# Performance work log

Hardware: AMD Instinct MI355X
Metric: run time of the kernel (lower is better)

Reference implementation:

```python
import jax, jax.numpy as jnp
import numpy as np

N_NODES = 100000
N_EDGES = 1600000
FEAT = 512
CLS = 64
HID = 200  # each hop layer output width; 3 hops -> 600 concat


def spmm(row, col, vals, x):
    # out[r] = sum_{e: row[e]==r} vals[e] * x[col[e]]  -- sparse A @ x
    return jax.ops.segment_sum(x[col] * vals[:, None], row, num_segments=x.shape[0])


def setup_inputs() -> dict:
    key = jax.random.key(0)
    ks = jax.random.split(key, 12)
    adj_index = jax.random.randint(ks[0], (2, N_EDGES), 0, N_NODES, dtype=jnp.int64)
    # scale like a normalized adjacency (~1/avg_degree) to keep powers stable
    adj_values = jax.random.uniform(ks[1], (N_EDGES,), dtype=jnp.float32) * (1.0 / 16.0)
    features = jax.random.normal(ks[2], (N_NODES, FEAT), dtype=jnp.float32)
    s1 = (2.0 / (FEAT + HID)) ** 0.5
    s2 = (2.0 / (3 * HID + HID)) ** 0.5
    sf = (2.0 / (3 * HID + CLS)) ** 0.5
    W1 = jax.random.normal(ks[3], (3, FEAT, HID), dtype=jnp.float32) * s1
    b1 = jax.random.normal(ks[4], (3, HID), dtype=jnp.float32) * 0.01
    W2 = jax.random.normal(ks[5], (3, 3 * HID, HID), dtype=jnp.float32) * s2
    b2 = jax.random.normal(ks[6], (3, HID), dtype=jnp.float32) * 0.01
    Wfc = jax.random.normal(ks[7], (3 * HID, CLS), dtype=jnp.float32) * sf
    bfc = jax.random.normal(ks[8], (CLS,), dtype=jnp.float32) * 0.01
    return {"adj_index": adj_index, "adj_values": adj_values, "features": features,
            "W1": W1, "b1": b1, "W2": W2, "b2": b2, "Wfc": Wfc, "bfc": bfc}


def reference(adj_index, adj_values, features, W1, b1, W2, b2, Wfc, bfc):
    # Inference mode: dropout is identity.
    row, col = adj_index[0], adj_index[1]
    # upper (sparse) layers: linear + bias + relu, then (iterations-1) spmm hops
    outs1 = []
    for i in range(3):  # iterations = i + 1
        h = jax.nn.relu(features @ W1[i] + b1[i][None, :])
        for _ in range(i):
            h = spmm(row, col, adj_values, h)
        outs1.append(h)
    abstract1 = jnp.concatenate(outs1, axis=1)  # [N, 600]
    # bottom (dense) layers: linear, (iterations-1) spmm hops, then + bias
    outs2 = []
    for i in range(3):
        h = abstract1 @ W2[i]
        for _ in range(i):
            h = spmm(row, col, adj_values, h)
        h = h + b2[i][None, :]
        outs2.append(h)
    abstract2 = jnp.concatenate(outs2, axis=1)  # [N, 600]
    node_emb = abstract2 @ Wfc + bfc  # [N, CLS]
    predictions = jax.nn.log_softmax(node_emb, axis=1)
    return node_emb, predictions
```

## Files before the change

### kernel.cpp

```cpp
#include <hip/hip_runtime.h>

typedef unsigned short u16;
typedef unsigned int u32;
typedef __attribute__((ext_vector_type(8))) short short8;
typedef __attribute__((ext_vector_type(4))) float f32x4;
typedef __attribute__((ext_vector_type(4))) u32 u32x4;
typedef __attribute__((ext_vector_type(2))) u32 u32x2;

#define NN 100000
#define PAD 640

__device__ __forceinline__ float b2f(u16 u) {
    union { u32 i; float f; } v; v.i = ((u32)u) << 16; return v.f;
}
__device__ __forceinline__ u16 f2b(float f) {
    union { float f; u32 i; } v; v.f = f;
    u32 x = v.i;
    return (u16)((x + 0x7FFFu + ((x >> 16) & 1u)) >> 16);
}
__device__ __forceinline__ u32 pack2(float lo, float hi) {
    return (u32)f2b(lo) | ((u32)f2b(hi) << 16);
}
__device__ __forceinline__ float rdf(const void* p, size_t i, int f) {
    return f ? ((const float*)p)[i] : b2f(((const u16*)p)[i]);
}
__device__ __forceinline__ void gload16(const u16* g, u16* l) {
    __builtin_amdgcn_global_load_lds(
        (const __attribute__((address_space(1))) void*)g,
        (__attribute__((address_space(3))) void*)l, 16, 0, 0);
}

__global__ void probe_k(const int* __restrict__ idx,
                        const void* avals, const void* feats, const void* W1,
                        const void* b1, const void* W2, const void* b2,
                        const void* Wfc, const void* bfc,
                        int* __restrict__ flags) {
    if (blockIdx.x != 0 || threadIdx.x >= 64) return;
    int lane = threadIdx.x;
    int v0 = idx[2 * lane + 1];
    int v1 = idx[2 * (lane + 64) + 1];
    int ok = (v0 == 0 && v1 == 0);
    int allz = __all(ok);
    if (lane == 0) flags[0] = allz ? 1 : 0;
    const void* ts[8] = {avals, feats, W1, b1, W2, b2, Wfc, bfc};
    const int ns[8] = {256, 256, 256, 128, 256, 128, 256, 32};
    for (int t = 0; t < 8; ++t) {
        const u16* p = (const u16*)ts[t];
        int n = ns[t], bad = 0;
        for (int i = lane; i < n; i += 64) {
            int e = (p[2 * i] >> 7) & 0xFF;
            if (e >= 133) bad++;
        }
        for (int off = 32; off; off >>= 1) bad += __shfl_xor(bad, off, 64);
        if (lane == 0) flags[1 + t] = (bad * 8 >= n) ? 1 : 0;
    }
}

__device__ __forceinline__ int load_row(const int* idx, int E, int f, int e) {
    return f ? idx[2 * e] : idx[e];
}
__device__ __forceinline__ int load_col(const int* idx, int E, int f, int e) {
    return f ? idx[2 * E + 2 * e] : idx[E + e];
}

__global__ void featconv_k(const void* __restrict__ src, u16* __restrict__ dst,
                           const int* __restrict__ flags) {
    int i = blockIdx.x * 256 + threadIdx.x;
    if (i >= NN * 64) return;
    int f = flags[2];
    size_t b = (size_t)i * 8;
    short8 o;
    if (f) {
        const float* sf = (const float*)src + b;
        f32x4 x0 = *(const f32x4*)sf;
        f32x4 x1 = *(const f32x4*)(sf + 4);
#pragma unroll
        for (int q = 0; q < 4; ++q) {
            o[q] = (short)f2b(x0[q]);
            o[q + 4] = (short)f2b(x1[q]);
        }
    } else {
        o = *(const short8*)((const u16*)src + b);
    }
    *(short8*)(dst + b) = o;
}

__global__ void prep_k(const void* __restrict__ W1, const void* __restrict__ W2,
                       const void* __restrict__ Wfc,
                       const void* __restrict__ b1, const void* __restrict__ b2,
                       const void* __restrict__ bfc,
                       u16* __restrict__ w1t, u16* __restrict__ w2t,
                       u16* __restrict__ wfct, float* __restrict__ biasf,
                       const int* __restrict__ flags) {
    int i = blockIdx.x * 256 + threadIdx.x;
    int job = blockIdx.y;
    if (job == 0) {
        if (i >= 640 * 512) return;
        int n = i >> 9, k = i & 511;
        float v = 0.f;
        if (n < 600) {
            int ib = n / 200, c = n % 200;
            v = rdf(W1, (size_t)ib * 102400 + (size_t)k * 200 + c, flags[3]);
        }
        w1t[i] = f2b(v);
    } else if (job == 1) {
        if (i >= 640 * 640) return;
        int n = i / 640, k = i % 640;
        float v = 0.f;
        if (n < 600 && k < 600) {
            int ib = n / 200, c = n % 200;
            v = rdf(W2, (size_t)ib * 120000 + (size_t)k * 200 + c, flags[5]);
        }
        w2t[i] = f2b(v);
    } else if (job == 2) {
        if (i >= 64 * 640) return;
        int n = i / 640, k = i % 640;
        float v = 0.f;
        if (k < 600) v = rdf(Wfc, (size_t)k * 64 + n, flags[7]);
        wfct[i] = f2b(v);
    } else if (job == 3) {
        if (i < 600) biasf[i] = rdf(b1, i, flags[4]);
        else if (i < 1200) biasf[i] = rdf(b2, i - 600, flags[6]);
        else if (i < 1264) biasf[i] = rdf(bfc, i - 1200, flags[8]);
    } else {
        if (i >= 64) return;
        int fb2 = flags[6], fwf = flags[7];
        float s = rdf(bfc, i, flags[8]);
        for (int k = 0; k < 200; ++k)
            s += rdf(b2, k, fb2) * rdf(Wfc, (size_t)k * 64 + i, fwf);
        biasf[1280 + i] = s;
    }
}

__device__ __forceinline__ int pad8(int c) { return (c + 7) & ~7; }

__global__ void count_k(const int* __restrict__ idx, int E, const int* __restrict__ flags,
                        int* __restrict__ counts) {
    int e = blockIdx.x * 256 + threadIdx.x;
    if (e >= E) return;
    int r = load_row(idx, E, flags[0], e);
    if ((u32)r >= NN) return;
    atomicAdd(&counts[r], 1);
}

__global__ void chunksum_k(const int* __restrict__ counts, int* __restrict__ chsum) {
    __shared__ int sm[256];
    int c = blockIdx.x, t = threadIdx.x;
    int base = c * 1024, s = 0;
    for (int i = t; i < 1024; i += 256) {
        int g = base + i;
        if (g < NN) s += pad8(counts[g]);
    }
    sm[t] = s; __syncthreads();
    for (int off = 128; off; off >>= 1) {
        if (t < off) sm[t] += sm[t + off];
        __syncthreads();
    }
    if (t == 0) chsum[c] = sm[0];
}

__global__ void chscan_k(const int* __restrict__ chsum, int nch, int* __restrict__ choff,
                         int* __restrict__ row_ptr, int E) {
    if (threadIdx.x == 0 && blockIdx.x == 0) {
        int run = 0;
        for (int c = 0; c < nch; ++c) { choff[c] = run; run += chsum[c]; }
        row_ptr[NN] = run;
    }
}

__global__ __launch_bounds__(1024) void scan_k(const int* __restrict__ counts,
                                               const int* __restrict__ choff,
                                               int* __restrict__ row_ptr,
                                               int* __restrict__ cursor) {
    __shared__ int sm[1024];
    int c = blockIdx.x, t = threadIdx.x;
    int g = c * 1024 + t;
    int v = (g < NN) ? pad8(counts[g]) : 0;
    sm[t] = v;
    __syncthreads();
    for (int off = 1; off < 1024; off <<= 1) {
        int add = (t >= off) ? sm[t - off] : 0;
        __syncthreads();
        sm[t] += add;
        __syncthreads();
    }
    if (g < NN) {
        int ex = choff[c] + sm[t] - v;
        row_ptr[g] = ex;
        cursor[g] = ex;
    }
}

__global__ void scatter_k(const int* __restrict__ idx, const void* __restrict__ avals, int E,
                          const int* __restrict__ flags, int* __restrict__ cursor,
                          int* __restrict__ edges) {
    int e = blockIdx.x * 256 + threadIdx.x;
    if (e >= E) return;
    int f = flags[0];
    int r = load_row(idx, E, f, e);
    if ((u32)r >= NN) return;
    int c = load_col(idx, E, f, e);
    if ((u32)c >= NN) c = 0;
    int p = atomicAdd(&cursor[r], 1);
    edges[2 * p] = c;
    ((float*)edges)[2 * p + 1] = rdf(avals, e, flags[1]);
}

__global__ void padfill_k(const int* __restrict__ cursor, const int* __restrict__ row_ptr,
                          int* __restrict__ edges) {
    int r = blockIdx.x * 256 + threadIdx.x;
    if (r >= NN) return;
    int p = cursor[r], e = row_ptr[r + 1];
    for (; p < e; ++p) {
        edges[2 * p] = 0;
        ((float*)edges)[2 * p + 1] = 0.f;
    }
}

__global__ __launch_bounds__(256) void gemm128_k(
    const u16* __restrict__ A, const u16* __restrict__ Bt,
    u16* __restrict__ C, float* __restrict__ Cf,
    const float* __restrict__ bias, int bias_n, int relu,
    int M, int K, int lda, int ldc) {
    __shared__ u16 As[128 * 32];
    __shared__ u16 Bs[128 * 32];
    const int tid = threadIdx.x;
    const int wave = tid >> 6, lane = tid & 63;

    const int nwg = gridDim.x;
    const int q = nwg >> 3, r8 = nwg & 7;
    const int xcd = blockIdx.x & 7, lo = blockIdx.x >> 3;
    const int wg = (xcd < r8 ? xcd * (q + 1) : r8 * (q + 1) + (xcd - r8) * q) + lo;
    const int bmi = wg / 5, bni = wg - bmi * 5;
    const int bm = bmi * 128, bn = bni * 128;

    const int wrow = (wave >> 1) * 64, wcol = (wave & 1) * 64;
    const int l15 = lane & 15, l4 = lane >> 4;
    f32x4 acc[4][4] = {};

    const int c0 = wave * 2;
    const int rowA0 = c0 * 16 + (lane >> 2);
    const int rowA1 = rowA0 + 16;
    const int colE = (lane & 3) * 8;
    int gr0 = bm + rowA0; if (gr0 >= M) gr0 = M - 1;
    int gr1 = bm + rowA1; if (gr1 >= M) gr1 = M - 1;
    const u16* a0p = A + (size_t)gr0 * lda + colE;
    const u16* a1p = A + (size_t)gr1 * lda + colE;
    const u16* b0p = Bt + (size_t)(bn + rowA0) * K + colE;
    const u16* b1p = Bt + (size_t)(bn + rowA1) * K + colE;
    u16* lA0 = As + c0 * 512;
    u16* lA1 = As + c0 * 512 + 512;
    u16* lB0 = Bs + c0 * 512;
    u16* lB1 = Bs + c0 * 512 + 512;

    for (int k0 = 0; k0 < K; k0 += 32) {
        __syncthreads();
        gload16(a0p + k0, lA0);
        gload16(a1p + k0, lA1);
        gload16(b0p + k0, lB0);
        gload16(b1p + k0, lB1);
        __syncthreads();
        short8 af[4], bf[4];
#pragma unroll
        for (int t = 0; t < 4; ++t) {
            af[t] = *(const short8*)&As[(wrow + t * 16 + l15) * 32 + l4 * 8];
            bf[t] = *(const short8*)&Bs[(wcol + t * 16 + l15) * 32 + l4 * 8];
        }
#pragma unroll
        for (int mi = 0; mi < 4; ++mi)
#pragma unroll
            for (int ni = 0; ni < 4; ++ni)
                acc[mi][ni] = __builtin_amdgcn_mfma_f32_16x16x32_bf16(
                    af[mi], bf[ni], acc[mi][ni], 0, 0, 0);
    }

#pragma unroll
    for (int mi = 0; mi < 4; ++mi)
#pragma unroll
        for (int ni = 0; ni < 4; ++ni)
#pragma unroll
            for (int r4 = 0; r4 < 4; ++r4) {
                int row = bm + wrow + mi * 16 + l4 * 4 + r4;
                int col = bn + wcol + ni * 16 + l15;
                if (row < M) {
                    float v = acc[mi][ni][r4];
                    if (bias && col < bias_n) v += bias[col];
                    if (relu) v = fmaxf(v, 0.0f);
                    if (C) C[(size_t)row * ldc + col] = f2b(v);
                    if (Cf) Cf[(size_t)row * ldc + col] = v;
                }
            }
}

__global__ __launch_bounds__(256) void fc64_k(
    const u16* __restrict__ A0, const u16* __restrict__ A1,
    const u16* __restrict__ Bt,
    float* __restrict__ out_ne, float* __restrict__ out_pred,
    const float* __restrict__ bias, int M, int K, int lda) {
    __shared__ __align__(16) char ldsbuf[128 * 64 * 4];
    u16* As = (u16*)ldsbuf;
    u16* Bs = (u16*)(ldsbuf + 8192);
    float* smC = (float*)ldsbuf;

    const int tid = threadIdx.x;
    const int wave = tid >> 6, lane = tid & 63;
    const int bm = blockIdx.x * 128;
    const int wrow = (wave >> 1) * 64, wcol = (wave & 1) * 32;
    const int l15 = lane & 15, l4 = lane >> 4;
    f32x4 acc[4][2] = {};

    const int colE = (lane & 3) * 8;
    int gr0 = bm + wave * 32 + (lane >> 2); if (gr0 >= M) gr0 = M - 1;
    int gr1 = bm + wave * 32 + 16 + (lane >> 2); if (gr1 >= M) gr1 = M - 1;
    const u16* a0p0 = A0 + (size_t)gr0 * lda + colE;
    const u16* a0p1 = A1 + (size_t)gr0 * lda + colE;
    const u16* a1p0 = A0 + (size_t)gr1 * lda + colE;
    const u16* a1p1 = A1 + (size_t)gr1 * lda + colE;
    const u16* bp = Bt + (size_t)(wave * 16 + (lane >> 2)) * K + colE;
    u16* lA0 = As + wave * 1024;
    u16* lA1 = As + wave * 1024 + 512;
    u16* lB = Bs + wave * 512;

    for (int k0 = 0; k0 < K; k0 += 32) {
        const bool in0 = (k0 + colE) < 200;
        const u16* pa0 = in0 ? a0p0 : a0p1;
        const u16* pa1 = in0 ? a1p0 : a1p1;
        __syncthreads();
        gload16(pa0 + k0, lA0);
        gload16(pa1 + k0, lA1);
        gload16(bp + k0, lB);
        __syncthreads();
        short8 af[4], bf[2];
#pragma unroll
        for (int t = 0; t < 4; ++t)
            af[t] = *(const short8*)&As[(wrow + t * 16 + l15) * 32 + l4 * 8];
#pragma unroll
        for (int t = 0; t < 2; ++t)
            bf[t] = *(const short8*)&Bs[(wcol + t * 16 + l15) * 32 + l4 * 8];
#pragma unroll
        for (int mi = 0; mi < 4; ++mi)
#pragma unroll
            for (int ni = 0; ni < 2; ++ni)
                acc[mi][ni] = __builtin_amdgcn_mfma_f32_16x16x32_bf16(
                    af[mi], bf[ni], acc[mi][ni], 0, 0, 0);
    }

    __syncthreads();
#pragma unroll
    for (int mi = 0; mi < 4; ++mi)
#pragma unroll
        for (int ni = 0; ni < 2; ++ni)
#pragma unroll
            for (int r4 = 0; r4 < 4; ++r4) {
                int rl = wrow + mi * 16 + l4 * 4 + r4;
                int col = wcol + ni * 16 + l15;
                int row = bm + rl;
                float v = acc[mi][ni][r4] + bias[col];
                smC[rl * 64 + col] = v;
                if (row < M) out_ne[(size_t)row * 64 + col] = v;
            }
    __syncthreads();

    const int rl = tid >> 1, half = tid & 1;
    const int row = bm + rl;
    float vv[32];
#pragma unroll
    for (int k = 0; k < 32; ++k) {
        int c = half * 32 + ((k + rl) & 31);
        vv[k] = smC[rl * 64 + c];
    }
    float m = vv[0];
#pragma unroll
    for (int k = 1; k < 32; ++k) m = fmaxf(m, vv[k]);
    m = fmaxf(m, __shfl_xor(m, 1, 64));
    float s = 0.f;
#pragma unroll
    for (int k = 0; k < 32; ++k) s += expf(vv[k] - m);
    s += __shfl_xor(s, 1, 64);
    float lg = m + logf(s);
    if (row < M) {
#pragma unroll
        for (int k = 0; k < 32; ++k) {
            int c = half * 32 + ((k + rl) & 31);
            out_pred[(size_t)row * 64 + c] = vv[k] - lg;
        }
    }
}

__global__ __launch_bounds__(256) void spmm400_k(
    const int* __restrict__ row_ptr, const int* __restrict__ edges,
    const u16* __restrict__ X, u16* __restrict__ Y1, u16* __restrict__ Yt,
    const float* __restrict__ bias1) {
    int r = blockIdx.x * 4 + (threadIdx.x >> 6);
    if (r >= NN) return;
    int lane = threadIdx.x & 63;
    int s = row_ptr[r], e = row_ptr[r + 1];
    if (s < 0) s = 0;
    if (e < s) e = s;
    float a[8] = {0.f, 0.f, 0.f, 0.f, 0.f, 0.f, 0.f, 0.f};
    const bool act = lane < 50;
    const u32* xl = (const u32*)X + lane * 4;
    for (int i = s; i < e; i += 8) {
        int cc[8]; float vv[8];
#pragma unroll
        for (int j = 0; j < 4; ++j) {
            u32x4 p = *(const u32x4*)(edges + 2 * (size_t)(i + 2 * j));
            union { u32 u; float f; } w0, w1;
            cc[2 * j] = (int)p[0];     w0.u = p[1];
            cc[2 * j + 1] = (int)p[2]; w1.u = p[3];
            vv[2 * j] = w0.f; vv[2 * j + 1] = w1.f;
        }
        if (act) {
            u32x4 g[8];
#pragma unroll
            for (int j = 0; j < 8; ++j) {
                u32 c = (u32)cc[j]; if (c >= NN) c = 0;
                g[j] = *(const u32x4*)(xl + (size_t)c * 320);
            }
#pragma unroll
            for (int j = 0; j < 8; ++j) {
                float v = vv[j];
#pragma unroll
                for (int q = 0; q < 4; ++q) {
                    union { u32 i; float f; } lo, hi;
                    lo.i = g[j][q] << 16; hi.i = g[j][q] & 0xffff0000u;
                    a[2 * q] = fmaf(v, lo.f, a[2 * q]);
                    a[2 * q + 1] = fmaf(v, hi.f, a[2 * q + 1]);
                }
            }
        }
    }
    if (bias1 && lane < 25) {
#pragma unroll
        for (int q = 0; q < 8; ++q) a[q] += bias1[lane * 8 + q];
    }
    u32x4 o;
    o[0] = pack2(a[0], a[1]); o[1] = pack2(a[2], a[3]);
    o[2] = pack2(a[4], a[5]); o[3] = pack2(a[6], a[7]);
    if (lane < 25) {
        *(u32x4*)((u32*)Y1 + (size_t)r * 320 + lane * 4) = o;
    } else if (lane < 50) {
        *(u32x4*)((u32*)Yt + (size_t)r * 100 + (lane - 25) * 4) = o;
    }
}

__global__ __launch_bounds__(256) void spmm200_k(
    const int* __restrict__ row_ptr, const int* __restrict__ edges,
    const u16* __restrict__ X, int ldx,
    u16* __restrict__ Y, int ldy,
    const float* __restrict__ bias) {
    int r = blockIdx.x * 4 + (threadIdx.x >> 6);
    if (r >= NN) return;
    int lane = threadIdx.x & 63;
    int s = row_ptr[r], e = row_ptr[r + 1];
    if (s < 0) s = 0;
    if (e < s) e = s;
    float a[4] = {0.f, 0.f, 0.f, 0.f};
    const bool act = lane < 50;
    const int ldxw = ldx >> 1, ldyw = ldy >> 1;
    const u32* xl = (const u32*)X + lane * 2;
    for (int i = s; i < e; i += 8) {
        int cc[8]; float vv[8];
#pragma unroll
        for (int j = 0; j < 4; ++j) {
            u32x4 p = *(const u32x4*)(edges + 2 * (size_t)(i + 2 * j));
            union { u32 u; float f; } w0, w1;
            cc[2 * j] = (int)p[0];     w0.u = p[1];
            cc[2 * j + 1] = (int)p[2]; w1.u = p[3];
            vv[2 * j] = w0.f; vv[2 * j + 1] = w1.f;
        }
        if (act) {
            u32x2 g[8];
#pragma unroll
            for (int j = 0; j < 8; ++j) {
                u32 c = (u32)cc[j]; if (c >= NN) c = 0;
                g[j] = *(const u32x2*)(xl + (size_t)c * ldxw);
            }
#pragma unroll
            for (int j = 0; j < 8; ++j) {
                float v = vv[j];
#pragma unroll
                for (int q = 0; q < 2; ++q) {
                    union { u32 i; float f; } lo, hi;
                    lo.i = g[j][q] << 16; hi.i = g[j][q] & 0xffff0000u;
                    a[2 * q] = fmaf(v, lo.f, a[2 * q]);
                    a[2 * q + 1] = fmaf(v, hi.f, a[2 * q + 1]);
                }
            }
        }
    }
    if (bias && act) {
#pragma unroll
        for (int q = 0; q < 4; ++q) a[q] += bias[lane * 4 + q];
    }
    if (act) {
        u32x2 o;
        o[0] = pack2(a[0], a[1]); o[1] = pack2(a[2], a[3]);
        *(u32x2*)((u32*)Y + (size_t)r * ldyw + lane * 2) = o;
    }
}

__global__ void copypad_k(const u16* __restrict__ src, u16* __restrict__ dst) {
    int i = blockIdx.x * 256 + threadIdx.x;
    if (i >= NN * 120) return;
    int r = i / 120, c = i % 120;
    if (c < 100)
        ((u32*)dst)[(size_t)r * 320 + c] = ((const u32*)src)[(size_t)r * 320 + c];
    else
        ((u32*)dst)[(size_t)r * 320 + 300 + (c - 100)] = 0u;
}

extern "C" void kernel_launch(void* const* d_in, const int* in_sizes, int n_in,
                              void* d_out, int out_size, void* d_ws, size_t ws_size,
                              hipStream_t stream) {
    const int* adj_idx = (const int*)d_in[0];
    const void* adj_vals = d_in[1];
    const void* feats = d_in[2];
    const void* W1 = d_in[3];
    const void* b1 = d_in[4];
    const void* W2 = d_in[5];
    const void* b2 = d_in[6];
    const void* Wfc = d_in[7];
    const void* bfc = d_in[8];
    const int E = in_sizes[1];
    (void)n_in; (void)out_size; (void)ws_size;

    char* ws = (char*)d_ws;
    size_t off = 0;
    auto alloc = [&](size_t b) { size_t o = off; off += (b + 255) & ~(size_t)255; return o; };
    u16* buf0 = (u16*)(ws + alloc((size_t)NN * PAD * 2));
    u16* buf1 = (u16*)(ws + alloc((size_t)NN * PAD * 2));
    u16* hop = (u16*)(ws + alloc((size_t)NN * 200 * 2));
    u16* w1t = (u16*)(ws + alloc((size_t)640 * 512 * 2));
    u16* w2t = (u16*)(ws + alloc((size_t)640 * 640 * 2));
    u16* wfct = (u16*)(ws + alloc((size_t)64 * 640 * 2));
    float* biasf = (float*)(ws + alloc(1344 * 4));
    int* counts = (int*)(ws + alloc((size_t)NN * 4));
    int* cursor = (int*)(ws + alloc((size_t)NN * 4));
    int* row_ptr = (int*)(ws + alloc((size_t)(NN + 1) * 4));
    int* chsum = (int*)(ws + alloc(4096));
    int* choff = (int*)(ws + alloc(4096));
    int* flags = (int*)(ws + alloc(256));
    int* edgesS = (int*)(ws + alloc(((size_t)E + 8 * (size_t)NN) * 8));

    u16* featsB = buf1;
    float* out_ne = (float*)d_out;
    float* out_pred = out_ne + (size_t)NN * 64;

    probe_k<<<1, 64, 0, stream>>>(adj_idx, adj_vals, feats, W1, b1, W2, b2, Wfc, bfc, flags);
    featconv_k<<<(NN * 64 + 255) / 256, 256, 0, stream>>>(feats, featsB, flags);
    dim3 gp(1600, 5);
    prep_k<<<gp, 256, 0, stream>>>(W1, W2, Wfc, b1, b2, bfc, w1t, w2t, wfct, biasf, flags);

    hipMemsetAsync(counts, 0, NN * 4, stream);
    count_k<<<(E + 255) / 256, 256, 0, stream>>>(adj_idx, E, flags, counts);
    const int NCH = (NN + 1023) / 1024;
    chunksum_k<<<NCH, 256, 0, stream>>>(counts, chsum);
    chscan_k<<<1, 64, 0, stream>>>(chsum, NCH, choff, row_ptr, E);
    scan_k<<<NCH, 1024, 0, stream>>>(counts, choff, row_ptr, cursor);
    scatter_k<<<(E + 255) / 256, 256, 0, stream>>>(adj_idx, adj_vals, E, flags, cursor, edgesS);
    padfill_k<<<(NN + 255) / 256, 256, 0, stream>>>(cursor, row_ptr, edgesS);

    const int NWG = ((NN + 127) / 128) * 5;
    gemm128_k<<<NWG, 256, 0, stream>>>(featsB, w1t, buf0, nullptr, biasf, 600, 1, NN, 512, 512, PAD);
    copypad_k<<<(NN * 120 + 255) / 256, 256, 0, stream>>>(buf0, buf1);
    spmm400_k<<<(NN + 3) / 4, 256, 0, stream>>>(row_ptr, edgesS,
                                                buf0 + 200, buf1 + 200, hop, nullptr);
    spmm200_k<<<(NN + 3) / 4, 256, 0, stream>>>(row_ptr, edgesS,
                                                hop, 200, buf1 + 400, PAD, nullptr);
    gemm128_k<<<NWG, 256, 0, stream>>>(buf1, w2t, buf0, nullptr, nullptr, 0, 0, NN, PAD, PAD, PAD);
    spmm400_k<<<(NN + 3) / 4, 256, 0, stream>>>(row_ptr, edgesS,
                                                buf0 + 200, buf1 + 200, hop, biasf + 800);
    spmm200_k<<<(NN + 3) / 4, 256, 0, stream>>>(row_ptr, edgesS,
                                                hop, 200, buf1 + 400, PAD, biasf + 1000);
    fc64_k<<<(NN + 127) / 128, 256, 0, stream>>>(buf0, buf1, wfct, out_ne, out_pred,
                                                 biasf + 1280, NN, PAD, PAD);
}
```

Measured before the change: 1.566 ms.

## Fuse feature conversion and pad copy into first GEMM

Drops the standalone fp32-to-bf16 feature conversion kernel and the copypad kernel. A new first-layer GEMM reads the raw features, converts them to bf16 in registers before staging them in LDS, and writes the relu output to both buffers for the needed column ranges. This removes a full write and reread of the 100k×512 bf16 feature matrix plus one 600-column copy pass. The cost is a GEMM whose A-operand load is now synchronous and unpipelined, with doubled global reads in fp32, and a scalar per-element epilogue store.

```diff
diff --git a/kernel.cpp b/kernel.cpp
--- a/kernel.cpp
+++ b/kernel.cpp
@@ -63,28 +63,6 @@
     return f ? idx[2 * E + 2 * e] : idx[E + e];
 }
 
-__global__ void featconv_k(const void* __restrict__ src, u16* __restrict__ dst,
-                           const int* __restrict__ flags) {
-    int i = blockIdx.x * 256 + threadIdx.x;
-    if (i >= NN * 64) return;
-    int f = flags[2];
-    size_t b = (size_t)i * 8;
-    short8 o;
-    if (f) {
-        const float* sf = (const float*)src + b;
-        f32x4 x0 = *(const f32x4*)sf;
-        f32x4 x1 = *(const f32x4*)(sf + 4);
-#pragma unroll
-        for (int q = 0; q < 4; ++q) {
-            o[q] = (short)f2b(x0[q]);
-            o[q + 4] = (short)f2b(x1[q]);
-        }
-    } else {
-        o = *(const short8*)((const u16*)src + b);
-    }
-    *(short8*)(dst + b) = o;
-}
-
 __global__ void prep_k(const void* __restrict__ W1, const void* __restrict__ W2,
                        const void* __restrict__ Wfc,
                        const void* __restrict__ b1, const void* __restrict__ b2,
@@ -217,6 +195,101 @@
     }
 }
 
+__global__ __launch_bounds__(256) void gemm1_k(
+    const void* __restrict__ A, const u16* __restrict__ Bt,
+    u16* __restrict__ C, u16* __restrict__ Cc,
+    const float* __restrict__ bias, const int* __restrict__ flags,
+    int M, int K, int lda, int ldc) {
+    __shared__ u16 As[128 * 32];
+    __shared__ u16 Bs[128 * 32];
+    const int tid = threadIdx.x;
+    const int wave = tid >> 6, lane = tid & 63;
+
+    const int nwg = gridDim.x;
+    const int q = nwg >> 3, r8 = nwg & 7;
+    const int xcd = blockIdx.x & 7, lo = blockIdx.x >> 3;
+    const int wg = (xcd < r8 ? xcd * (q + 1) : r8 * (q + 1) + (xcd - r8) * q) + lo;
+    const int bmi = wg / 5, bni = wg - bmi * 5;
+    const int bm = bmi * 128, bn = bni * 128;
+
+    const int wrow = (wave >> 1) * 64, wcol = (wave & 1) * 64;
+    const int l15 = lane & 15, l4 = lane >> 4;
+    f32x4 acc[4][4] = {};
+
+    const int ff = flags[2];
+    const int c0 = wave * 2;
+    const int rowA0 = c0 * 16 + (lane >> 2);
+    const int rowA1 = rowA0 + 16;
+    const int colE = (lane & 3) * 8;
+    int gr0 = bm + rowA0; if (gr0 >= M) gr0 = M - 1;
+    int gr1 = bm + rowA1; if (gr1 >= M) gr1 = M - 1;
+    const float* a0f = (const float*)A + (size_t)gr0 * lda + colE;
+    const float* a1f = (const float*)A + (size_t)gr1 * lda + colE;
+    const u16* a0h = (const u16*)A + (size_t)gr0 * lda + colE;
+    const u16* a1h = (const u16*)A + (size_t)gr1 * lda + colE;
+    const u16* b0p = Bt + (size_t)(bn + rowA0) * K + colE;
+    const u16* b1p = Bt + (size_t)(bn + rowA1) * K + colE;
+    u16* lA0 = &As[rowA0 * 32 + colE];
+    u16* lA1 = &As[rowA1 * 32 + colE];
+    u16* lB0 = Bs + c0 * 512;
+    u16* lB1 = Bs + c0 * 512 + 512;
+
+    for (int k0 = 0; k0 < K; k0 += 32) {
+        short8 av0, av1;
+        if (ff) {
+            f32x4 x0 = *(const f32x4*)(a0f + k0);
+            f32x4 x1 = *(const f32x4*)(a0f + k0 + 4);
+            f32x4 y0 = *(const f32x4*)(a1f + k0);
+            f32x4 y1 = *(const f32x4*)(a1f + k0 + 4);
+#pragma unroll
+            for (int t = 0; t < 4; ++t) {
+                av0[t] = (short)f2b(x0[t]); av0[t + 4] = (short)f2b(x1[t]);
+                av1[t] = (short)f2b(y0[t]); av1[t + 4] = (short)f2b(y1[t]);
+            }
+        } else {
+            av0 = *(const short8*)(a0h + k0);
+            av1 = *(const short8*)(a1h + k0);
+        }
+        __syncthreads();
+        *(short8*)lA0 = av0;
+        *(short8*)lA1 = av1;
+        gload16(b0p + k0, lB0);
+        gload16(b1p + k0, lB1);
+        __syncthreads();
+        short8 af[4], bf[4];
+#pragma unroll
+        for (int t = 0; t < 4; ++t) {
+            af[t] = *(const short8*)&As[(wrow + t * 16 + l15) * 32 + l4 * 8];
+            bf[t] = *(const short8*)&Bs[(wcol + t * 16 + l15) * 32 + l4 * 8];
+        }
+#pragma unroll
+        for (int mi = 0; mi < 4; ++mi)
+#pragma unroll
+            for (int ni = 0; ni < 4; ++ni)
+                acc[mi][ni] = __builtin_amdgcn_mfma_f32_16x16x32_bf16(
+                    af[mi], bf[ni], acc[mi][ni], 0, 0, 0);
+    }
+
+#pragma unroll
+    for (int mi = 0; mi < 4; ++mi)
+#pragma unroll
+        for (int ni = 0; ni < 4; ++ni)
+#pragma unroll
+            for (int r4 = 0; r4 < 4; ++r4) {
+                int row = bm + wrow + mi * 16 + l4 * 4 + r4;
+                int col = bn + wcol + ni * 16 + l15;
+                if (row < M) {
+                    float v = acc[mi][ni][r4];
+                    if (col < 600) v += bias[col];
+                    v = fmaxf(v, 0.0f);
+                    u16 b = f2b(v);
+                    C[(size_t)row * ldc + col] = b;
+                    if (col < 200 || col >= 600)
+                        Cc[(size_t)row * ldc + col] = b;
+                }
+            }
+}
+
 __global__ __launch_bounds__(256) void gemm128_k(
     const u16* __restrict__ A, const u16* __restrict__ Bt,
     u16* __restrict__ C, float* __restrict__ Cf,
@@ -500,16 +573,6 @@
     }
 }
 
-__global__ void copypad_k(const u16* __restrict__ src, u16* __restrict__ dst) {
-    int i = blockIdx.x * 256 + threadIdx.x;
-    if (i >= NN * 120) return;
-    int r = i / 120, c = i % 120;
-    if (c < 100)
-        ((u32*)dst)[(size_t)r * 320 + c] = ((const u32*)src)[(size_t)r * 320 + c];
-    else
-        ((u32*)dst)[(size_t)r * 320 + 300 + (c - 100)] = 0u;
-}
-
 extern "C" void kernel_launch(void* const* d_in, const int* in_sizes, int n_in,
                               void* d_out, int out_size, void* d_ws, size_t ws_size,
                               hipStream_t stream) {
@@ -543,12 +606,10 @@
     int* flags = (int*)(ws + alloc(256));
     int* edgesS = (int*)(ws + alloc(((size_t)E + 8 * (size_t)NN) * 8));
 
-    u16* featsB = buf1;
     float* out_ne = (float*)d_out;
     float* out_pred = out_ne + (size_t)NN * 64;
 
     probe_k<<<1, 64, 0, stream>>>(adj_idx, adj_vals, feats, W1, b1, W2, b2, Wfc, bfc, flags);
-    featconv_k<<<(NN * 64 + 255) / 256, 256, 0, stream>>>(feats, featsB, flags);
     dim3 gp(1600, 5);
     prep_k<<<gp, 256, 0, stream>>>(W1, W2, Wfc, b1, b2, bfc, w1t, w2t, wfct, biasf, flags);
 
@@ -562,8 +623,7 @@
     padfill_k<<<(NN + 255) / 256, 256, 0, stream>>>(cursor, row_ptr, edgesS);
 
     const int NWG = ((NN + 127) / 128) * 5;
-    gemm128_k<<<NWG, 256, 0, stream>>>(featsB, w1t, buf0, nullptr, biasf, 600, 1, NN, 512, 512, PAD);
-    copypad_k<<<(NN * 120 + 255) / 256, 256, 0, stream>>>(buf0, buf1);
+    gemm1_k<<<NWG, 256, 0, stream>>>(feats, w1t, buf0, buf1, biasf, flags, NN, 512, 512, PAD);
     spmm400_k<<<(NN + 3) / 4, 256, 0, stream>>>(row_ptr, edgesS,
                                                 buf0 + 200, buf1 + 200, hop, nullptr);
     spmm200_k<<<(NN + 3) / 4, 256, 0, stream>>>(row_ptr, edgesS,
```

Result: faster. 1.521 ms (-2.9%).
